# Optimization experiments

Measured on AMD Instinct MI355X. Metric: run time of the kernel, lower is better.

Reference implementation:

```python
import jax, jax.numpy as jnp
import numpy as np

B, T, E, H, V = 64, 512, 512, 1024, 32000
PADDING_TOKEN = 0


def setup_inputs() -> dict:
    key = jax.random.key(0)
    k0, k1, k2, k3, k4, k5 = jax.random.split(key, 6)
    history = jax.random.randint(k0, (B, T), 0, V)
    emb = jax.random.normal(k1, (V, E), dtype=jnp.float32) * 0.02
    emb = emb.at[PADDING_TOKEN].set(0.0)  # padding_idx=0 row is zeros
    s = 1.0 / np.sqrt(H).astype(np.float32)
    # PyTorch RNNCell layout: weight_ih [H, E], weight_hh [H, H]; bias=False
    W_ih = jax.random.uniform(k2, (H, E), jnp.float32, -s, s)
    W_hh = jax.random.uniform(k3, (H, H), jnp.float32, -s, s)
    # nn.Linear(hidden, vocab): weight [V, H], bias [V]
    sc = 1.0 / np.sqrt(H).astype(np.float32)
    W_cls = jax.random.uniform(k4, (V, H), jnp.float32, -sc, sc)
    b_cls = jax.random.uniform(k5, (V,), jnp.float32, -sc, sc)
    return {"history": history, "emb": emb, "W_ih": W_ih, "W_hh": W_hh,
            "W_cls": W_cls, "b_cls": b_cls}


def reference(history, emb, W_ih, W_hh, W_cls, b_cls):
    x = emb[history]                                  # [B, T, E]
    # Precompute all input projections in one big GEMM: [B, T, H]
    xi = jnp.einsum('bte,he->bth', x, W_ih)
    h0 = jnp.zeros((x.shape[0], W_hh.shape[0]), dtype=x.dtype)

    def step(h, xt):                                  # xt: [B, H]
        h_new = jnp.tanh(xt + h @ W_hh.T)
        return h_new, None

    h_final, _ = jax.lax.scan(step, h0, jnp.swapaxes(xi, 0, 1))  # scan over T
    logits = h_final @ W_cls.T + b_cls                # [B, V]
    return logits, h_final
```

## Files before the change

kernel.cpp:

```cpp
#include <hip/hip_runtime.h>
#include <hip/hip_bf16.h>
#include <cstdint>
#include <cstddef>

#define B_ 64
#define T_ 512
#define E_ 512
#define H_ 1024
#define V_ 32000
#define BK 64

typedef __attribute__((ext_vector_type(8))) short bf16x8;
typedef __attribute__((ext_vector_type(4))) float f32x4;
typedef __attribute__((ext_vector_type(4))) float float4_t;
typedef unsigned long long ull;
typedef unsigned int u32;

static __device__ __forceinline__ unsigned short f2b(float f) {
  union { float f; u32 u; } v; v.f = f;
  u32 u = v.u;
  u32 r = (u + 0x7FFFu + ((u >> 16) & 1u)) >> 16;
  return (unsigned short)r;
}
static __device__ __forceinline__ float b2f(unsigned short s) {
  union { u32 u; float f; } v; v.u = ((u32)s) << 16;
  return v.f;
}
static __device__ __forceinline__ bf16x8 cvt8(const float* p) {
  bf16x8 r;
#pragma unroll
  for (int i = 0; i < 8; i++) r[i] = (short)f2b(p[i]);
  return r;
}
static __device__ __forceinline__ ull ald(const ull* p) {
  return __hip_atomic_load(p, __ATOMIC_RELAXED, __HIP_MEMORY_SCOPE_AGENT);
}
static __device__ __forceinline__ u32 ald32(const u32* p) {
  return __hip_atomic_load(p, __ATOMIC_RELAXED, __HIP_MEMORY_SCOPE_AGENT);
}
static __device__ __forceinline__ void ast64(ull* p, ull v) {
  __hip_atomic_store(p, v, __ATOMIC_RELAXED, __HIP_MEMORY_SCOPE_AGENT);
}
static __device__ __forceinline__ void ast32(u32* p, u32 v) {
  __hip_atomic_store(p, v, __ATOMIC_RELAXED, __HIP_MEMORY_SCOPE_AGENT);
}
static __device__ __forceinline__ int swz128(int row, int byte_off) {
  return row * 128 + (byte_off ^ ((row & 7) << 4));
}

#define NFLAGS 256

__global__ void k_init(u32* flags) {
  int i = threadIdx.x;
  if (i < NFLAGS) ast32(&flags[i], 0u);
}

__global__ __launch_bounds__(256)
void k_e2(const float* __restrict__ emb, const float* __restrict__ Wih,
          unsigned short* __restrict__ E2) {
  __shared__ unsigned char As[64 * 128];
  __shared__ unsigned char Bs[64 * 128];
  const int tid = threadIdx.x;
  const int lane = tid & 63;
  const int w = tid >> 6;
  const int n0 = blockIdx.x * 64;
  const int m0 = blockIdx.y * 64;
  f32x4 acc[4];
#pragma unroll
  for (int i = 0; i < 4; i++) acc[i] = (f32x4)0.0f;

  for (int kc = 0; kc < E_ / BK; kc++) {
    const int k0 = kc * BK;
    __syncthreads();
#pragma unroll
    for (int it = 0; it < 2; it++) {
      int idx = tid + it * 256;
      int r = idx >> 3;
      int k = (idx & 7) * 8;
      float tmp[8];
      *(float4_t*)(tmp)     = *(const float4_t*)(emb + (size_t)(m0 + r) * E_ + k0 + k);
      *(float4_t*)(tmp + 4) = *(const float4_t*)(emb + (size_t)(m0 + r) * E_ + k0 + k + 4);
      *(bf16x8*)(As + swz128(r, k * 2)) = cvt8(tmp);
      *(float4_t*)(tmp)     = *(const float4_t*)(Wih + (size_t)(n0 + r) * E_ + k0 + k);
      *(float4_t*)(tmp + 4) = *(const float4_t*)(Wih + (size_t)(n0 + r) * E_ + k0 + k + 4);
      *(bf16x8*)(Bs + swz128(r, k * 2)) = cvt8(tmp);
    }
    __syncthreads();
#pragma unroll
    for (int kk = 0; kk < 2; kk++) {
      int kb = kk * 64 + (lane >> 4) * 16;
      bf16x8 a = *(const bf16x8*)(As + swz128(w * 16 + (lane & 15), kb));
#pragma unroll
      for (int nt = 0; nt < 4; nt++) {
        bf16x8 b = *(const bf16x8*)(Bs + swz128(nt * 16 + (lane & 15), kb));
        acc[nt] = __builtin_amdgcn_mfma_f32_16x16x32_bf16(a, b, acc[nt], 0, 0, 0);
      }
    }
  }
#pragma unroll
  for (int nt = 0; nt < 4; nt++) {
#pragma unroll
    for (int reg = 0; reg < 4; reg++) {
      int row = m0 + w * 16 + (lane >> 4) * 4 + reg;
      int col = n0 + nt * 16 + (lane & 15);
      E2[(size_t)row * H_ + col] = f2b(acc[nt][reg]);
    }
  }
}

__global__ __launch_bounds__(512, 1)
void k_scan(const int* __restrict__ hist, const float* __restrict__ Whh,
            const unsigned short* __restrict__ E2,
            unsigned short* __restrict__ hb0, unsigned short* __restrict__ hb1,
            u32* __restrict__ flags, float* __restrict__ out_h) {
  const int tid = threadIdx.x;
  const int lane = tid & 63;
  const int w = tid >> 6;
  const int bid = blockIdx.x;
  const int g = bid & 7;
  const int j = bid >> 3;
  const int row0 = g * 8;
  const int wcol0 = j * 128 + w * 16;

  __shared__ unsigned char hs[8 * 2048];

  const int ar = lane & 15;
  const int a7 = ar & 7;
  const int hi = lane >> 4;

  bf16x8 Wreg[32];
  {
    const float* wrow = Whh + (size_t)(wcol0 + ar) * H_ + hi * 8;
#pragma unroll
    for (int kk = 0; kk < 32; kk++) {
      float tmp[8];
      *(float4_t*)(tmp)     = *(const float4_t*)(wrow + kk * 32);
      *(float4_t*)(tmp + 4) = *(const float4_t*)(wrow + kk * 32 + 4);
      Wreg[kk] = cvt8(tmp);
    }
  }

  u32* gflags = flags + g * 16;

  for (int t = 0; t < T_; t++) {
    const unsigned short* hc = (t & 1) ? hb1 : hb0;
    unsigned short*       hn = (t & 1) ? hb0 : hb1;

    float xiv[4];
    {
      const int tok = hist[(size_t)(row0 + a7) * T_ + t];
      const ull xw = *(const ull*)(E2 + (size_t)tok * H_ + wcol0 + hi * 4);
      xiv[0] = b2f((unsigned short)xw);
      xiv[1] = b2f((unsigned short)(xw >> 16));
      xiv[2] = b2f((unsigned short)(xw >> 32));
      xiv[3] = b2f((unsigned short)(xw >> 48));
    }

    f32x4 acc0 = (f32x4)0.0f, acc1 = (f32x4)0.0f;

    if (t > 0) {
      const u32 e = (u32)t;
      for (;;) {
        u32 f = ald32(&gflags[lane & 7]);
        if (__all(f >= e)) break;
        __builtin_amdgcn_s_sleep(1);
      }
      asm volatile("" ::: "memory");

      {
        const ull* hrow = (const ull*)(hc + (size_t)(row0 + w) * H_);
        ull h0 = ald(hrow + lane);
        ull h1 = ald(hrow + lane + 64);
        ull h2 = ald(hrow + lane + 128);
        ull h3 = ald(hrow + lane + 192);
        unsigned char* hsb = hs + w * 2048;
        const int sw = w << 4;
        *(ull*)(hsb + ((lane * 8)        ^ sw)) = h0;
        *(ull*)(hsb + ((lane * 8 + 512)  ^ sw)) = h1;
        *(ull*)(hsb + ((lane * 8 + 1024) ^ sw)) = h2;
        *(ull*)(hsb + ((lane * 8 + 1536) ^ sw)) = h3;
      }
      __syncthreads();

      const unsigned char* brow = hs + a7 * 2048;
      const int swb = a7 << 4;
#pragma unroll
      for (int kk = 0; kk < 32; kk += 2) {
        bf16x8 b0 = *(const bf16x8*)(brow + (((kk)     * 64 + hi * 16) ^ swb));
        bf16x8 b1 = *(const bf16x8*)(brow + (((kk + 1) * 64 + hi * 16) ^ swb));
        acc0 = __builtin_amdgcn_mfma_f32_16x16x32_bf16(Wreg[kk],     b0, acc0, 0, 0, 0);
        acc1 = __builtin_amdgcn_mfma_f32_16x16x32_bf16(Wreg[kk + 1], b1, acc1, 0, 0, 0);
      }
    }

    if (ar < 8) {
      float hval[4];
#pragma unroll
      for (int reg = 0; reg < 4; reg++)
        hval[reg] = tanhf(acc0[reg] + acc1[reg] + xiv[reg]);
      ull hw = (ull)f2b(hval[0]) | ((ull)f2b(hval[1]) << 16) |
               ((ull)f2b(hval[2]) << 32) | ((ull)f2b(hval[3]) << 48);
      ast64((ull*)(hn + (size_t)(row0 + ar) * H_ + wcol0 + hi * 4), hw);
      if (t == T_ - 1) {
        float4_t o = {hval[0], hval[1], hval[2], hval[3]};
        *(float4_t*)(out_h + (size_t)(row0 + ar) * H_ + wcol0 + hi * 4) = o;
      }
    }

    asm volatile("s_waitcnt vmcnt(0)" ::: "memory");
    __syncthreads();
    if (tid == 0)
      ast32(&gflags[j], (u32)(t + 1));
  }
}

__global__ __launch_bounds__(256)
void k_logits(const unsigned short* __restrict__ hb,
              const float* __restrict__ Wcls, const float* __restrict__ bcls,
              float* __restrict__ out) {
  __shared__ unsigned char Bs[64 * 128];
  const int tid = threadIdx.x;
  const int lane = tid & 63;
  const int w = tid >> 6;
  const int n0 = blockIdx.x * 64;
  f32x4 acc[4];
#pragma unroll
  for (int i = 0; i < 4; i++) acc[i] = (f32x4)0.0f;

  for (int kc = 0; kc < H_ / BK; kc++) {
    const int k0 = kc * BK;
    __syncthreads();
#pragma unroll
    for (int it = 0; it < 2; it++) {
      int idx = tid + it * 256;
      int r = idx >> 3;
      int k = (idx & 7) * 8;
      float tmp[8];
      *(float4_t*)(tmp)     = *(const float4_t*)(Wcls + (size_t)(n0 + r) * H_ + k0 + k);
      *(float4_t*)(tmp + 4) = *(const float4_t*)(Wcls + (size_t)(n0 + r) * H_ + k0 + k + 4);
      *(bf16x8*)(Bs + swz128(r, k * 2)) = cvt8(tmp);
    }
    __syncthreads();
#pragma unroll
    for (int kk = 0; kk < 2; kk++) {
      const unsigned short* ap =
          hb + (size_t)(w * 16 + (lane & 15)) * H_ + k0 + kk * 32 + (lane >> 4) * 8;
      bf16x8 a = *(const bf16x8*)ap;
      int kb = kk * 64 + (lane >> 4) * 16;
#pragma unroll
      for (int nt = 0; nt < 4; nt++) {
        bf16x8 b = *(const bf16x8*)(Bs + swz128(nt * 16 + (lane & 15), kb));
        acc[nt] = __builtin_amdgcn_mfma_f32_16x16x32_bf16(a, b, acc[nt], 0, 0, 0);
      }
    }
  }
#pragma unroll
  for (int nt = 0; nt < 4; nt++) {
    int col = n0 + nt * 16 + (lane & 15);
    float bias = bcls[col];
#pragma unroll
    for (int reg = 0; reg < 4; reg++) {
      int row = w * 16 + (lane >> 4) * 4 + reg;
      out[(size_t)row * V_ + col] = acc[nt][reg] + bias;
    }
  }
}

extern "C" void kernel_launch(void* const* d_in, const int* in_sizes, int n_in,
                              void* d_out, int out_size, void* d_ws, size_t ws_size,
                              hipStream_t stream) {
  const int*   hist = (const int*)d_in[0];
  const float* emb  = (const float*)d_in[1];
  const float* Wih  = (const float*)d_in[2];
  const float* Whh  = (const float*)d_in[3];
  const float* Wcls = (const float*)d_in[4];
  const float* bcls = (const float*)d_in[5];
  float* out = (float*)d_out;

  unsigned char* ws = (unsigned char*)d_ws;
  const size_t E2_BYTES = (size_t)V_ * H_ * 2;
  const size_t HB_BYTES = (size_t)B_ * H_ * 2;
  unsigned short* E2    = (unsigned short*)ws;
  unsigned short* hb0   = (unsigned short*)(ws + E2_BYTES);
  unsigned short* hb1   = (unsigned short*)(ws + E2_BYTES + HB_BYTES);
  u32*            flags = (u32*)(ws + E2_BYTES + 2 * HB_BYTES);

  k_init<<<1, 256, 0, stream>>>(flags);
  k_e2<<<dim3(16, 500), 256, 0, stream>>>(emb, Wih, E2);
  k_scan<<<64, 512, 0, stream>>>(hist, Whh, E2, hb0, hb1, flags,
                                 out + (size_t)B_ * V_);
  k_logits<<<500, 256, 0, stream>>>(hb0, Wcls, bcls, out);
}
```

Baseline: 1.634 ms.

## Replace per-step flag barrier with tagged hidden-state words in triple buffer

Each bf16 hidden value is now stored in a 32-bit word with the timestep in the upper half. Consumers poll the data directly until every tag matches the expected step, instead of waiting on per-block flags. This drops the per-step vmcnt wait, the block barrier and the flag store/poll round trip, and uses three rotating buffers so writers cannot overwrite data still being read. The cost is doubled hidden-state traffic, more load work inside the spin loop, and a larger zero-init kernel.

```diff
diff --git a/kernel.cpp b/kernel.cpp
--- a/kernel.cpp
+++ b/kernel.cpp
@@ -35,9 +35,6 @@
 static __device__ __forceinline__ ull ald(const ull* p) {
   return __hip_atomic_load(p, __ATOMIC_RELAXED, __HIP_MEMORY_SCOPE_AGENT);
 }
-static __device__ __forceinline__ u32 ald32(const u32* p) {
-  return __hip_atomic_load(p, __ATOMIC_RELAXED, __HIP_MEMORY_SCOPE_AGENT);
-}
 static __device__ __forceinline__ void ast64(ull* p, ull v) {
   __hip_atomic_store(p, v, __ATOMIC_RELAXED, __HIP_MEMORY_SCOPE_AGENT);
 }
@@ -48,11 +45,9 @@
   return row * 128 + (byte_off ^ ((row & 7) << 4));
 }
 
-#define NFLAGS 256
-
-__global__ void k_init(u32* flags) {
-  int i = threadIdx.x;
-  if (i < NFLAGS) ast32(&flags[i], 0u);
+__global__ void k_init(u32* xb) {
+  int i = blockIdx.x * blockDim.x + threadIdx.x;
+  ast32(xb + i, 0u);
 }
 
 __global__ __launch_bounds__(256)
@@ -111,8 +106,8 @@
 __global__ __launch_bounds__(512, 1)
 void k_scan(const int* __restrict__ hist, const float* __restrict__ Whh,
             const unsigned short* __restrict__ E2,
-            unsigned short* __restrict__ hb0, unsigned short* __restrict__ hb1,
-            u32* __restrict__ flags, float* __restrict__ out_h) {
+            u32* __restrict__ xb,
+            unsigned short* __restrict__ hbf, float* __restrict__ out_h) {
   const int tid = threadIdx.x;
   const int lane = tid & 63;
   const int w = tid >> 6;
@@ -140,12 +135,7 @@
     }
   }
 
-  u32* gflags = flags + g * 16;
-
   for (int t = 0; t < T_; t++) {
-    const unsigned short* hc = (t & 1) ? hb1 : hb0;
-    unsigned short*       hn = (t & 1) ? hb0 : hb1;
-
     float xiv[4];
     {
       const int tok = hist[(size_t)(row0 + a7) * T_ + t];
@@ -159,26 +149,29 @@
     f32x4 acc0 = (f32x4)0.0f, acc1 = (f32x4)0.0f;
 
     if (t > 0) {
-      const u32 e = (u32)t;
+      const u32* rbuf = xb + (size_t)((t + 2) % 3) * (B_ * H_);
+      const ull* src = (const ull*)(rbuf + (size_t)(row0 + w) * H_);
+      const u32 tagv = (u32)t << 16;
+      ull hv[8];
       for (;;) {
-        u32 f = ald32(&gflags[lane & 7]);
-        if (__all(f >= e)) break;
+#pragma unroll
+        for (int i = 0; i < 8; i++) hv[i] = ald(src + lane + 64 * i);
+        u32 bad = 0;
+#pragma unroll
+        for (int i = 0; i < 8; i++)
+          bad |= (((u32)hv[i] ^ tagv) | ((u32)(hv[i] >> 32) ^ tagv)) &
+                 0xFFFF0000u;
+        if (__all(bad == 0)) break;
         __builtin_amdgcn_s_sleep(1);
       }
-      asm volatile("" ::: "memory");
-
       {
-        const ull* hrow = (const ull*)(hc + (size_t)(row0 + w) * H_);
-        ull h0 = ald(hrow + lane);
-        ull h1 = ald(hrow + lane + 64);
-        ull h2 = ald(hrow + lane + 128);
-        ull h3 = ald(hrow + lane + 192);
         unsigned char* hsb = hs + w * 2048;
         const int sw = w << 4;
-        *(ull*)(hsb + ((lane * 8)        ^ sw)) = h0;
-        *(ull*)(hsb + ((lane * 8 + 512)  ^ sw)) = h1;
-        *(ull*)(hsb + ((lane * 8 + 1024) ^ sw)) = h2;
-        *(ull*)(hsb + ((lane * 8 + 1536) ^ sw)) = h3;
+#pragma unroll
+        for (int i = 0; i < 8; i++) {
+          u32 p = ((u32)hv[i] & 0xFFFFu) | ((u32)(hv[i] >> 32) << 16);
+          *(u32*)(hsb + ((lane * 4 + i * 256) ^ sw)) = p;
+        }
       }
       __syncthreads();
 
@@ -198,19 +191,21 @@
 #pragma unroll
       for (int reg = 0; reg < 4; reg++)
         hval[reg] = tanhf(acc0[reg] + acc1[reg] + xiv[reg]);
-      ull hw = (ull)f2b(hval[0]) | ((ull)f2b(hval[1]) << 16) |
-               ((ull)f2b(hval[2]) << 32) | ((ull)f2b(hval[3]) << 48);
-      ast64((ull*)(hn + (size_t)(row0 + ar) * H_ + wcol0 + hi * 4), hw);
+      const u32 tagw = (u32)(t + 1) << 16;
+      ull lo = (ull)(tagw | f2b(hval[0])) | ((ull)(tagw | f2b(hval[1])) << 32);
+      ull hi2 = (ull)(tagw | f2b(hval[2])) | ((ull)(tagw | f2b(hval[3])) << 32);
+      u32* wbuf = xb + (size_t)(t % 3) * (B_ * H_);
+      ull* dst = (ull*)(wbuf + (size_t)(row0 + ar) * H_ + wcol0 + hi * 4);
+      ast64(dst, lo);
+      ast64(dst + 1, hi2);
       if (t == T_ - 1) {
         float4_t o = {hval[0], hval[1], hval[2], hval[3]};
         *(float4_t*)(out_h + (size_t)(row0 + ar) * H_ + wcol0 + hi * 4) = o;
-      }
-    }
-
-    asm volatile("s_waitcnt vmcnt(0)" ::: "memory");
-    __syncthreads();
-    if (tid == 0)
-      ast32(&gflags[j], (u32)(t + 1));
+        unsigned short* hp = hbf + (size_t)(row0 + ar) * H_ + wcol0 + hi * 4;
+        hp[0] = f2b(hval[0]); hp[1] = f2b(hval[1]);
+        hp[2] = f2b(hval[2]); hp[3] = f2b(hval[3]);
+      }
+    }
   }
 }
 
@@ -279,15 +274,14 @@
 
   unsigned char* ws = (unsigned char*)d_ws;
   const size_t E2_BYTES = (size_t)V_ * H_ * 2;
-  const size_t HB_BYTES = (size_t)B_ * H_ * 2;
-  unsigned short* E2    = (unsigned short*)ws;
-  unsigned short* hb0   = (unsigned short*)(ws + E2_BYTES);
-  unsigned short* hb1   = (unsigned short*)(ws + E2_BYTES + HB_BYTES);
-  u32*            flags = (u32*)(ws + E2_BYTES + 2 * HB_BYTES);
-
-  k_init<<<1, 256, 0, stream>>>(flags);
+  const size_t XB_BYTES = (size_t)3 * B_ * H_ * 4;
+  unsigned short* E2  = (unsigned short*)ws;
+  u32*            xbf = (u32*)(ws + E2_BYTES);
+  unsigned short* hbf = (unsigned short*)(ws + E2_BYTES + XB_BYTES);
+
+  k_init<<<768, 256, 0, stream>>>(xbf);
   k_e2<<<dim3(16, 500), 256, 0, stream>>>(emb, Wih, E2);
-  k_scan<<<64, 512, 0, stream>>>(hist, Whh, E2, hb0, hb1, flags,
+  k_scan<<<64, 512, 0, stream>>>(hist, Whh, E2, xbf, hbf,
                                  out + (size_t)B_ * V_);
-  k_logits<<<500, 256, 0, stream>>>(hb0, Wcls, bcls, out);
-}
+  k_logits<<<500, 256, 0, stream>>>(hbf, Wcls, bcls, out);
+}
```

Measured after the change: 1.518 ms. 7.1% less time.
